# Kernel tuning notes

Measured on AMD Instinct MI355X. Metric: run time of the kernel, lower is better.

Reference implementation:

```python
import jax, jax.numpy as jnp
import numpy as np

N_NODES = 100000
N_EDGES = 640000
N_GRAPHS = 512
NODE_IN, EDGE_IN, HID, L = 64, 16, 128, 4
BN_EPS = 1e-5


def setup_inputs() -> dict:
    key = jax.random.key(0)
    ks = jax.random.split(key, 20)
    inp = {
        "x": jax.random.normal(ks[0], (N_NODES, NODE_IN), jnp.float32),
        "edge_index": jax.random.randint(ks[1], (2, N_EDGES), 0, N_NODES, jnp.int64 if jax.config.jax_enable_x64 else jnp.int32),
        "edge_attr": jax.random.normal(ks[2], (N_EDGES, EDGE_IN), jnp.float32),
        "batch": jnp.sort(jax.random.randint(ks[3], (N_NODES,), 0, N_GRAPHS)),
        # projections
        "node_w": jax.random.normal(ks[4], (NODE_IN, HID), jnp.float32) / np.sqrt(NODE_IN),
        "node_b": jnp.zeros((HID,), jnp.float32),
        "edge_w": jax.random.normal(ks[5], (EDGE_IN, HID), jnp.float32) / np.sqrt(EDGE_IN),
        "edge_b": jnp.zeros((HID,), jnp.float32),
        # per-layer GINE MLP: Linear(HID,2H) -> ReLU -> Linear(2H,HID)
        "w1": jax.random.normal(ks[6], (L, HID, 2 * HID), jnp.float32) / np.sqrt(HID),
        "b1": jnp.zeros((L, 2 * HID), jnp.float32),
        "w2": jax.random.normal(ks[7], (L, 2 * HID, HID), jnp.float32) / np.sqrt(2 * HID),
        "b2": jnp.zeros((L, HID), jnp.float32),
        # batchnorm affine params
        "gamma": jnp.ones((L, HID), jnp.float32),
        "beta": jnp.zeros((L, HID), jnp.float32),
    }
    return inp


def reference(x, edge_index, edge_attr, batch, node_w, node_b, edge_w, edge_b,
              w1, b1, w2, b2, gamma, beta):
    n = x.shape[0]
    h = jax.nn.relu(x @ node_w + node_b)              # [N, H]
    e = jax.nn.relu(edge_attr @ edge_w + edge_b)      # [E, H]
    src, dst = edge_index[0], edge_index[1]
    for l in range(L):
        # GINEConv: msg = relu(x_src + edge_attr); sum-aggregate at dst; eps = 0
        msg = jax.nn.relu(h[src] + e)                 # [E, H]
        agg = jax.ops.segment_sum(msg, dst, num_segments=n)
        z = h + agg                                   # (1+eps)*x + aggr
        z = jax.nn.relu(z @ w1[l] + b1[l]) @ w2[l] + b2[l]
        # BatchNorm1d (training-mode batch stats, biased var)
        mean = jnp.mean(z, axis=0)
        var = jnp.var(z, axis=0)
        z = (z - mean) * jax.lax.rsqrt(var + BN_EPS) * gamma[l] + beta[l]
        h = jax.nn.relu(z)                            # dropout is identity at eval
    # global mean pool over graphs
    sums = jax.ops.segment_sum(h, batch, num_segments=N_GRAPHS)
    cnt = jax.ops.segment_sum(jnp.ones((n,), h.dtype), batch, num_segments=N_GRAPHS)
    return sums / jnp.maximum(cnt, 1.0)[:, None]      # [G, H]
```

## Files before the change

kernel.cpp:

```cpp
#include <hip/hip_runtime.h>
#include <hip/hip_bf16.h>

#define NN 100000
#define NE 640000
#define NG 512
#define NIN 64
#define EIN 16
#define H 128
#define H2 256
#define NL 4

__global__ __launch_bounds__(256) void k_node_proj(const float* __restrict__ x,
                                                   const float* __restrict__ W,
                                                   const float* __restrict__ b,
                                                   float* __restrict__ h) {
    __shared__ float sW[NIN * H];
    int tid = threadIdx.x;
    for (int i = tid; i < NIN * H; i += 256) sW[i] = W[i];
    __syncthreads();
    int c = tid & 127, half = tid >> 7;
    for (int node = blockIdx.x * 2 + half; node < NN; node += gridDim.x * 2) {
        const float* xr = x + (size_t)node * NIN;
        float acc = b[c];
#pragma unroll
        for (int k = 0; k < NIN; ++k) acc = fmaf(xr[k], sW[k * H + c], acc);
        h[(size_t)node * H + c] = fmaxf(acc, 0.f);
    }
}

__global__ __launch_bounds__(256) void k_hist(const int* __restrict__ dst, int* __restrict__ deg) {
    int e = blockIdx.x * 256 + threadIdx.x;
    if (e < NE) atomicAdd(&deg[dst[e]], 1);
}

__global__ __launch_bounds__(256) void k_scan1(const int* __restrict__ deg, int* __restrict__ ex,
                                               int* __restrict__ totals) {
    __shared__ int s[256];
    int t = threadIdx.x, b = blockIdx.x;
    int base = b * 1024 + t * 4;
    int v0 = (base + 0 < NN) ? deg[base + 0] : 0;
    int v1 = (base + 1 < NN) ? deg[base + 1] : 0;
    int v2 = (base + 2 < NN) ? deg[base + 2] : 0;
    int v3 = (base + 3 < NN) ? deg[base + 3] : 0;
    int t0 = v0, t1 = t0 + v1, t2 = t1 + v2, tsum = t2 + v3;
    s[t] = tsum;
    __syncthreads();
#pragma unroll
    for (int d = 1; d < 256; d <<= 1) {
        int add = (t >= d) ? s[t - d] : 0;
        __syncthreads();
        s[t] += add;
        __syncthreads();
    }
    int excl = s[t] - tsum;
    ex[base + 0] = excl;
    ex[base + 1] = excl + t0;
    ex[base + 2] = excl + t1;
    ex[base + 3] = excl + t2;
    if (t == 255) totals[b] = s[t];
}

__global__ void k_scan2(const int* __restrict__ totals, int* __restrict__ boff) {
    __shared__ int s[256];
    int t = threadIdx.x;
    int v = (t < 98) ? totals[t] : 0;
    s[t] = v;
    __syncthreads();
#pragma unroll
    for (int d = 1; d < 256; d <<= 1) {
        int add = (t >= d) ? s[t - d] : 0;
        __syncthreads();
        s[t] += add;
        __syncthreads();
    }
    if (t < 98) boff[t] = s[t] - v;
}

__global__ __launch_bounds__(256) void k_scan3(const int* __restrict__ ex, const int* __restrict__ boff,
                                               int* __restrict__ rowptr, int* __restrict__ cursor) {
    int i = blockIdx.x * 256 + threadIdx.x;
    if (i < NN) {
        int r = ex[i] + boff[i >> 10];
        rowptr[i] = r;
        cursor[i] = r;
    }
    if (i == 0) rowptr[NN] = NE;
}

__global__ __launch_bounds__(256) void k_scatter(const int* __restrict__ dst, int* __restrict__ cursor,
                                                 int* __restrict__ eids) {
    int e = blockIdx.x * 256 + threadIdx.x;
    if (e < NE) {
        int p = atomicAdd(&cursor[dst[e]], 1);
        eids[p] = e;
    }
}

__global__ void k_prm_id(float* __restrict__ prm) {
    int c = threadIdx.x;
    prm[c] = 1.f;
    prm[H + c] = 0.f;
}

__global__ __launch_bounds__(256) void k_agg(const int* __restrict__ rowptr, const int* __restrict__ eids,
                                             const int* __restrict__ src, const float* __restrict__ ea,
                                             const float* __restrict__ We, const float* __restrict__ be,
                                             const float* __restrict__ hsrc, const float* __restrict__ prm,
                                             float* __restrict__ agg) {
    int tid = threadIdx.x;
    int c = tid & 127, grp = tid >> 7;
    float wcol[EIN];
#pragma unroll
    for (int k = 0; k < EIN; ++k) wcol[k] = We[k * H + c];
    float bec = be[c], sc = prm[c], sh = prm[H + c];
    int nb = blockIdx.x * 8;
#pragma unroll
    for (int rep = 0; rep < 4; ++rep) {
        int n = nb + rep * 2 + grp;
        int s0 = rowptr[n], s1 = rowptr[n + 1];
        float acc = 0.f;
        for (int idx = s0; idx < s1; ++idx) {
            int eid = eids[idx];
            int sv = src[eid];
            const float4* ear = (const float4*)(ea + (size_t)eid * EIN);
            float4 e0 = ear[0], e1 = ear[1], e2 = ear[2], e3 = ear[3];
            float p = bec;
            p = fmaf(e0.x, wcol[0], p);  p = fmaf(e0.y, wcol[1], p);
            p = fmaf(e0.z, wcol[2], p);  p = fmaf(e0.w, wcol[3], p);
            p = fmaf(e1.x, wcol[4], p);  p = fmaf(e1.y, wcol[5], p);
            p = fmaf(e1.z, wcol[6], p);  p = fmaf(e1.w, wcol[7], p);
            p = fmaf(e2.x, wcol[8], p);  p = fmaf(e2.y, wcol[9], p);
            p = fmaf(e2.z, wcol[10], p); p = fmaf(e2.w, wcol[11], p);
            p = fmaf(e3.x, wcol[12], p); p = fmaf(e3.y, wcol[13], p);
            p = fmaf(e3.z, wcol[14], p); p = fmaf(e3.w, wcol[15], p);
            p = fmaxf(p, 0.f);
            float hv = hsrc[(size_t)sv * H + c];
            hv = fmaxf(fmaf(sc, hv, sh), 0.f);
            acc += fmaxf(hv + p, 0.f);
        }
        agg[(size_t)n * H + c] = acc;
    }
}

__global__ __launch_bounds__(256) void k_mlp(const float* __restrict__ hsrc,
                                             const float* __restrict__ prm,
                                             float* __restrict__ agg,
                                             const float* __restrict__ w1,
                                             const float* __restrict__ b1,
                                             const float* __restrict__ w2,
                                             const float* __restrict__ b2,
                                             float* __restrict__ stats) {
    __shared__ float sz[32 * H];
    __shared__ float st[32 * H2];
    __shared__ float ls[2 * H];
    int tid = threadIdx.x;
    int base = blockIdx.x * 32;
    ls[tid < 256 ? tid : 0] = 0.f;

    float4* sz4 = (float4*)sz;
    const float4* X4 = (const float4*)hsrc;
    const float4* A4 = (const float4*)agg;
#pragma unroll
    for (int it = 0; it < 4; ++it) {
        int chunk = tid + it * 256;
        int n = chunk >> 5;
        int c4 = (chunk & 31);
        const float4 sc4 = *(const float4*)&prm[c4 * 4];
        const float4 sh4 = *(const float4*)&prm[H + c4 * 4];
        size_t gi = (size_t)(base + n) * 32 + c4;
        float4 hv = X4[gi], av = A4[gi];
        float4 z;
        z.x = fmaxf(fmaf(sc4.x, hv.x, sh4.x), 0.f) + av.x;
        z.y = fmaxf(fmaf(sc4.y, hv.y, sh4.y), 0.f) + av.y;
        z.z = fmaxf(fmaf(sc4.z, hv.z, sh4.z), 0.f) + av.z;
        z.w = fmaxf(fmaf(sc4.w, hv.w, sh4.w), 0.f) + av.w;
        sz4[chunk] = z;
    }
    __syncthreads();

    {
        int c64 = tid & 63, ng = tid >> 6;
        const float4* W14 = (const float4*)w1;
        float4 acc[8];
        float4 b1v = *(const float4*)&b1[c64 * 4];
#pragma unroll
        for (int n = 0; n < 8; ++n) acc[n] = b1v;
        for (int k0 = 0; k0 < H; k0 += 4) {
            float4 wv0 = W14[(k0 + 0) * 64 + c64];
            float4 wv1 = W14[(k0 + 1) * 64 + c64];
            float4 wv2 = W14[(k0 + 2) * 64 + c64];
            float4 wv3 = W14[(k0 + 3) * 64 + c64];
#pragma unroll
            for (int n = 0; n < 8; ++n) {
                float4 zv = sz4[(ng * 8 + n) * 32 + (k0 >> 2)];
                acc[n].x = fmaf(zv.x, wv0.x, acc[n].x); acc[n].y = fmaf(zv.x, wv0.y, acc[n].y);
                acc[n].z = fmaf(zv.x, wv0.z, acc[n].z); acc[n].w = fmaf(zv.x, wv0.w, acc[n].w);
                acc[n].x = fmaf(zv.y, wv1.x, acc[n].x); acc[n].y = fmaf(zv.y, wv1.y, acc[n].y);
                acc[n].z = fmaf(zv.y, wv1.z, acc[n].z); acc[n].w = fmaf(zv.y, wv1.w, acc[n].w);
                acc[n].x = fmaf(zv.z, wv2.x, acc[n].x); acc[n].y = fmaf(zv.z, wv2.y, acc[n].y);
                acc[n].z = fmaf(zv.z, wv2.z, acc[n].z); acc[n].w = fmaf(zv.z, wv2.w, acc[n].w);
                acc[n].x = fmaf(zv.w, wv3.x, acc[n].x); acc[n].y = fmaf(zv.w, wv3.y, acc[n].y);
                acc[n].z = fmaf(zv.w, wv3.z, acc[n].z); acc[n].w = fmaf(zv.w, wv3.w, acc[n].w);
            }
        }
        float4* st4 = (float4*)st;
#pragma unroll
        for (int n = 0; n < 8; ++n) {
            float4 r;
            r.x = fmaxf(acc[n].x, 0.f); r.y = fmaxf(acc[n].y, 0.f);
            r.z = fmaxf(acc[n].z, 0.f); r.w = fmaxf(acc[n].w, 0.f);
            st4[(ng * 8 + n) * 64 + c64] = r;
        }
    }
    __syncthreads();

    {
        int c32 = tid & 31, ng = tid >> 5;
        const float4* W24 = (const float4*)w2;
        const float4* st4 = (const float4*)st;
        float4 acc2[4];
        float4 b2v = *(const float4*)&b2[c32 * 4];
#pragma unroll
        for (int n = 0; n < 4; ++n) acc2[n] = b2v;
        for (int j0 = 0; j0 < H2; j0 += 4) {
            float4 wv0 = W24[(j0 + 0) * 32 + c32];
            float4 wv1 = W24[(j0 + 1) * 32 + c32];
            float4 wv2 = W24[(j0 + 2) * 32 + c32];
            float4 wv3 = W24[(j0 + 3) * 32 + c32];
#pragma unroll
            for (int n = 0; n < 4; ++n) {
                float4 tv = st4[(ng * 4 + n) * 64 + (j0 >> 2)];
                acc2[n].x = fmaf(tv.x, wv0.x, acc2[n].x); acc2[n].y = fmaf(tv.x, wv0.y, acc2[n].y);
                acc2[n].z = fmaf(tv.x, wv0.z, acc2[n].z); acc2[n].w = fmaf(tv.x, wv0.w, acc2[n].w);
                acc2[n].x = fmaf(tv.y, wv1.x, acc2[n].x); acc2[n].y = fmaf(tv.y, wv1.y, acc2[n].y);
                acc2[n].z = fmaf(tv.y, wv1.z, acc2[n].z); acc2[n].w = fmaf(tv.y, wv1.w, acc2[n].w);
                acc2[n].x = fmaf(tv.z, wv2.x, acc2[n].x); acc2[n].y = fmaf(tv.z, wv2.y, acc2[n].y);
                acc2[n].z = fmaf(tv.z, wv2.z, acc2[n].z); acc2[n].w = fmaf(tv.z, wv2.w, acc2[n].w);
                acc2[n].x = fmaf(tv.w, wv3.x, acc2[n].x); acc2[n].y = fmaf(tv.w, wv3.y, acc2[n].y);
                acc2[n].z = fmaf(tv.w, wv3.z, acc2[n].z); acc2[n].w = fmaf(tv.w, wv3.w, acc2[n].w);
            }
        }
        float4* O4 = (float4*)agg;
        float4 sv = {0, 0, 0, 0}, qv = {0, 0, 0, 0};
#pragma unroll
        for (int n = 0; n < 4; ++n) {
            O4[(size_t)(base + ng * 4 + n) * 32 + c32] = acc2[n];
            sv.x += acc2[n].x; sv.y += acc2[n].y; sv.z += acc2[n].z; sv.w += acc2[n].w;
            qv.x += acc2[n].x * acc2[n].x; qv.y += acc2[n].y * acc2[n].y;
            qv.z += acc2[n].z * acc2[n].z; qv.w += acc2[n].w * acc2[n].w;
        }
        int cb = c32 * 4;
        atomicAdd(&ls[cb + 0], sv.x); atomicAdd(&ls[cb + 1], sv.y);
        atomicAdd(&ls[cb + 2], sv.z); atomicAdd(&ls[cb + 3], sv.w);
        atomicAdd(&ls[H + cb + 0], qv.x); atomicAdd(&ls[H + cb + 1], qv.y);
        atomicAdd(&ls[H + cb + 2], qv.z); atomicAdd(&ls[H + cb + 3], qv.w);
    }
    __syncthreads();
    if (tid < 256) atomicAdd(&stats[tid], ls[tid]);
}

__global__ void k_bn_fin(const float* __restrict__ stats, const float* __restrict__ gamma,
                         const float* __restrict__ beta, float* __restrict__ prm) {
    int c = threadIdx.x;
    float mean = stats[c] * (1.f / NN);
    float var = stats[H + c] * (1.f / NN) - mean * mean;
    float sc = gamma[c] * rsqrtf(var + 1e-5f);
    prm[c] = sc;
    prm[H + c] = beta[c] - mean * sc;
}

__global__ __launch_bounds__(256) void k_pool(const float* __restrict__ z2, const float* __restrict__ prm,
                                              const int* __restrict__ batch, float* __restrict__ sums,
                                              float* __restrict__ cntf) {
    int tid = threadIdx.x;
    int c = tid & 127, half = tid >> 7;
    float sc = prm[c], sh = prm[H + c];
    int n0 = blockIdx.x * 64 + half * 32;
    float acc = 0.f;
    int curg = -1, runlen = 0;
    for (int i = 0; i < 32; ++i) {
        int n = n0 + i;
        if (n >= NN) break;
        int g = batch[n];
        float v = fmaxf(fmaf(sc, z2[(size_t)n * H + c], sh), 0.f);
        if (g != curg) {
            if (curg >= 0) {
                atomicAdd(&sums[(size_t)curg * H + c], acc);
                if (c == 0) atomicAdd(&cntf[curg], (float)runlen);
            }
            curg = g; acc = v; runlen = 1;
        } else {
            acc += v; runlen++;
        }
    }
    if (curg >= 0) {
        atomicAdd(&sums[(size_t)curg * H + c], acc);
        if (c == 0) atomicAdd(&cntf[curg], (float)runlen);
    }
}

__global__ void k_pool_fin(const float* __restrict__ sums, const float* __restrict__ cntf,
                           float* __restrict__ out) {
    int i = blockIdx.x * blockDim.x + threadIdx.x;
    if (i < NG * H) {
        int g = i >> 7;
        out[i] = sums[i] / fmaxf(cntf[g], 1.f);
    }
}

extern "C" void kernel_launch(void* const* d_in, const int* in_sizes, int n_in,
                              void* d_out, int out_size, void* d_ws, size_t ws_size,
                              hipStream_t stream) {
    const float* x      = (const float*)d_in[0];
    const int*   ei     = (const int*)d_in[1];
    const float* ea     = (const float*)d_in[2];
    const int*   batch  = (const int*)d_in[3];
    const float* node_w = (const float*)d_in[4];
    const float* node_b = (const float*)d_in[5];
    const float* edge_w = (const float*)d_in[6];
    const float* edge_b = (const float*)d_in[7];
    const float* w1     = (const float*)d_in[8];
    const float* b1     = (const float*)d_in[9];
    const float* w2     = (const float*)d_in[10];
    const float* b2     = (const float*)d_in[11];
    const float* gamma  = (const float*)d_in[12];
    const float* beta   = (const float*)d_in[13];
    float* out = (float*)d_out;

    char* ws = (char*)d_ws;
    const size_t SZ_H = (size_t)NN * H * 4;
    float* X     = (float*)(ws);
    float* Y     = (float*)(ws + SZ_H);
    char*  tail  = ws + 2 * SZ_H;
    float* stats = (float*)(tail);
    float* prm   = (float*)(tail + 1024);
    float* pool  = (float*)(tail + 1024 + 8192);
    float* cntf  = (float*)(tail + 1024 + 8192 + 262144);
    char*  itail = tail + 1024 + 8192 + 262144 + 2048;
    int* deg    = (int*)(itail);
    int* ex     = deg + 100352;
    int* totals = ex + 100352;
    int* boff   = totals + 128;
    int* rowptr = boff + 128;
    int* cursor = rowptr + 100352;
    int* eids   = cursor + 100352;

    const int* srcp = ei;
    const int* dstp = ei + NE;

    hipMemsetAsync(deg, 0, 100352 * sizeof(int), stream);
    k_hist<<<2500, 256, 0, stream>>>(dstp, deg);
    k_scan1<<<98, 256, 0, stream>>>(deg, ex, totals);
    k_scan2<<<1, 256, 0, stream>>>(totals, boff);
    k_scan3<<<392, 256, 0, stream>>>(ex, boff, rowptr, cursor);
    k_scatter<<<2500, 256, 0, stream>>>(dstp, cursor, eids);

    k_prm_id<<<1, 128, 0, stream>>>(prm);
    k_node_proj<<<2048, 256, 0, stream>>>(x, node_w, node_b, X);

    float* hs = X;
    float* ag = Y;
    for (int l = 0; l < NL; ++l) {
        hipMemsetAsync(stats, 0, 256 * sizeof(float), stream);
        k_agg<<<12500, 256, 0, stream>>>(rowptr, eids, srcp, ea, edge_w, edge_b,
                                         hs, prm + l * 256, ag);
        k_mlp<<<3125, 256, 0, stream>>>(hs, prm + l * 256, ag,
                                        w1 + (size_t)l * H * H2, b1 + (size_t)l * H2,
                                        w2 + (size_t)l * H2 * H, b2 + (size_t)l * H, stats);
        k_bn_fin<<<1, 128, 0, stream>>>(stats, gamma + (size_t)l * H, beta + (size_t)l * H,
                                        prm + (l + 1) * 256);
        float* tmp = hs; hs = ag; ag = tmp;
    }

    hipMemsetAsync(pool, 0, (NG * H + NG) * sizeof(float), stream);
    k_pool<<<1563, 256, 0, stream>>>(hs, prm + NL * 256, batch, pool, cntf);
    k_pool_fin<<<256, 256, 0, stream>>>(pool, cntf, out);
}
```

Measured before the change: 2.081 ms.

## Edge-balanced segmented aggregation with packed edge records and retiled MLP

Aggregation now splits the sorted edge list into fixed 32-edge chunks per thread group instead of walking one node's adjacency list at a time. This evens out load across degree-skewed nodes, and per-destination partial sums are flushed with atomics. Edge records now pack src, dst and edge id into one int4, removing the dependent eids→src load chain. Loads are batched four edges at a time to raise memory-level parallelism. The cost is an extra memset of the aggregation buffer each layer plus atomic traffic. The MLP kernel is also retiled so each thread covers 8 output columns, and the hidden tile is padded to avoid LDS bank conflicts.

```diff
diff --git a/kernel.cpp b/kernel.cpp
--- a/kernel.cpp
+++ b/kernel.cpp
@@ -9,6 +9,12 @@
 #define H 128
 #define H2 256
 #define NL 4
+
+#define FMA4(acc, s, wv)                      \
+    acc.x = fmaf(s, wv.x, acc.x);             \
+    acc.y = fmaf(s, wv.y, acc.y);             \
+    acc.z = fmaf(s, wv.z, acc.z);             \
+    acc.w = fmaf(s, wv.w, acc.w)
 
 __global__ __launch_bounds__(256) void k_node_proj(const float* __restrict__ x,
                                                    const float* __restrict__ W,
@@ -87,12 +93,15 @@
     if (i == 0) rowptr[NN] = NE;
 }
 
-__global__ __launch_bounds__(256) void k_scatter(const int* __restrict__ dst, int* __restrict__ cursor,
-                                                 int* __restrict__ eids) {
+__global__ __launch_bounds__(256) void k_scatter(const int* __restrict__ src,
+                                                 const int* __restrict__ dst,
+                                                 int* __restrict__ cursor,
+                                                 int4* __restrict__ erec) {
     int e = blockIdx.x * 256 + threadIdx.x;
     if (e < NE) {
-        int p = atomicAdd(&cursor[dst[e]], 1);
-        eids[p] = e;
+        int d = dst[e];
+        int p = atomicAdd(&cursor[d], 1);
+        erec[p] = make_int4(src[e], d, e, 0);
     }
 }
 
@@ -102,10 +111,12 @@
     prm[H + c] = 0.f;
 }
 
-__global__ __launch_bounds__(256) void k_agg(const int* __restrict__ rowptr, const int* __restrict__ eids,
-                                             const int* __restrict__ src, const float* __restrict__ ea,
-                                             const float* __restrict__ We, const float* __restrict__ be,
-                                             const float* __restrict__ hsrc, const float* __restrict__ prm,
+__global__ __launch_bounds__(256) void k_agg(const int4* __restrict__ erec,
+                                             const float* __restrict__ ea,
+                                             const float* __restrict__ We,
+                                             const float* __restrict__ be,
+                                             const float* __restrict__ hsrc,
+                                             const float* __restrict__ prm,
                                              float* __restrict__ agg) {
     int tid = threadIdx.x;
     int c = tid & 127, grp = tid >> 7;
@@ -113,35 +124,65 @@
 #pragma unroll
     for (int k = 0; k < EIN; ++k) wcol[k] = We[k * H + c];
     float bec = be[c], sc = prm[c], sh = prm[H + c];
-    int nb = blockIdx.x * 8;
-#pragma unroll
-    for (int rep = 0; rep < 4; ++rep) {
-        int n = nb + rep * 2 + grp;
-        int s0 = rowptr[n], s1 = rowptr[n + 1];
-        float acc = 0.f;
-        for (int idx = s0; idx < s1; ++idx) {
-            int eid = eids[idx];
-            int sv = src[eid];
-            const float4* ear = (const float4*)(ea + (size_t)eid * EIN);
-            float4 e0 = ear[0], e1 = ear[1], e2 = ear[2], e3 = ear[3];
-            float p = bec;
-            p = fmaf(e0.x, wcol[0], p);  p = fmaf(e0.y, wcol[1], p);
-            p = fmaf(e0.z, wcol[2], p);  p = fmaf(e0.w, wcol[3], p);
-            p = fmaf(e1.x, wcol[4], p);  p = fmaf(e1.y, wcol[5], p);
-            p = fmaf(e1.z, wcol[6], p);  p = fmaf(e1.w, wcol[7], p);
-            p = fmaf(e2.x, wcol[8], p);  p = fmaf(e2.y, wcol[9], p);
-            p = fmaf(e2.z, wcol[10], p); p = fmaf(e2.w, wcol[11], p);
-            p = fmaf(e3.x, wcol[12], p); p = fmaf(e3.y, wcol[13], p);
-            p = fmaf(e3.z, wcol[14], p); p = fmaf(e3.w, wcol[15], p);
-            p = fmaxf(p, 0.f);
-            float hv = hsrc[(size_t)sv * H + c];
-            hv = fmaxf(fmaf(sc, hv, sh), 0.f);
-            acc += fmaxf(hv + p, 0.f);
-        }
-        agg[(size_t)n * H + c] = acc;
-    }
-}
-
+    const float4* ea4 = (const float4*)ea;
+    int base = (blockIdx.x * 2 + grp) * 32;
+    int cur = erec[base].y;
+    float acc = 0.f;
+#pragma unroll 2
+    for (int i0 = 0; i0 < 32; i0 += 4) {
+        int4 r0 = erec[base + i0 + 0];
+        int4 r1 = erec[base + i0 + 1];
+        int4 r2 = erec[base + i0 + 2];
+        int4 r3 = erec[base + i0 + 3];
+        float hv0 = hsrc[(size_t)r0.x * H + c];
+        float hv1 = hsrc[(size_t)r1.x * H + c];
+        float hv2 = hsrc[(size_t)r2.x * H + c];
+        float hv3 = hsrc[(size_t)r3.x * H + c];
+        float4 a0 = ea4[(size_t)r0.z * 4 + 0], a1 = ea4[(size_t)r0.z * 4 + 1],
+               a2 = ea4[(size_t)r0.z * 4 + 2], a3 = ea4[(size_t)r0.z * 4 + 3];
+        float4 b0 = ea4[(size_t)r1.z * 4 + 0], b1 = ea4[(size_t)r1.z * 4 + 1],
+               b2 = ea4[(size_t)r1.z * 4 + 2], b3 = ea4[(size_t)r1.z * 4 + 3];
+        float4 c0 = ea4[(size_t)r2.z * 4 + 0], c1 = ea4[(size_t)r2.z * 4 + 1],
+               c2 = ea4[(size_t)r2.z * 4 + 2], c3 = ea4[(size_t)r2.z * 4 + 3];
+        float4 d0 = ea4[(size_t)r3.z * 4 + 0], d1 = ea4[(size_t)r3.z * 4 + 1],
+               d2 = ea4[(size_t)r3.z * 4 + 2], d3 = ea4[(size_t)r3.z * 4 + 3];
+
+#define EPROJ(pp, e0, e1, e2, e3)                                              \
+        {                                                                      \
+            pp = bec;                                                          \
+            pp = fmaf(e0.x, wcol[0], pp);  pp = fmaf(e0.y, wcol[1], pp);       \
+            pp = fmaf(e0.z, wcol[2], pp);  pp = fmaf(e0.w, wcol[3], pp);       \
+            pp = fmaf(e1.x, wcol[4], pp);  pp = fmaf(e1.y, wcol[5], pp);       \
+            pp = fmaf(e1.z, wcol[6], pp);  pp = fmaf(e1.w, wcol[7], pp);       \
+            pp = fmaf(e2.x, wcol[8], pp);  pp = fmaf(e2.y, wcol[9], pp);       \
+            pp = fmaf(e2.z, wcol[10], pp); pp = fmaf(e2.w, wcol[11], pp);      \
+            pp = fmaf(e3.x, wcol[12], pp); pp = fmaf(e3.y, wcol[13], pp);      \
+            pp = fmaf(e3.z, wcol[14], pp); pp = fmaf(e3.w, wcol[15], pp);      \
+            pp = fmaxf(pp, 0.f);                                               \
+        }
+        float p0, p1, p2, p3;
+        EPROJ(p0, a0, a1, a2, a3)
+        EPROJ(p1, b0, b1, b2, b3)
+        EPROJ(p2, c0, c1, c2, c3)
+        EPROJ(p3, d0, d1, d2, d3)
+#undef EPROJ
+        float m0 = fmaxf(fmaxf(fmaf(sc, hv0, sh), 0.f) + p0, 0.f);
+        float m1 = fmaxf(fmaxf(fmaf(sc, hv1, sh), 0.f) + p1, 0.f);
+        float m2 = fmaxf(fmaxf(fmaf(sc, hv2, sh), 0.f) + p2, 0.f);
+        float m3 = fmaxf(fmaxf(fmaf(sc, hv3, sh), 0.f) + p3, 0.f);
+        if (r0.y != cur) { atomicAdd(&agg[(size_t)cur * H + c], acc); acc = 0.f; cur = r0.y; }
+        acc += m0;
+        if (r1.y != cur) { atomicAdd(&agg[(size_t)cur * H + c], acc); acc = 0.f; cur = r1.y; }
+        acc += m1;
+        if (r2.y != cur) { atomicAdd(&agg[(size_t)cur * H + c], acc); acc = 0.f; cur = r2.y; }
+        acc += m2;
+        if (r3.y != cur) { atomicAdd(&agg[(size_t)cur * H + c], acc); acc = 0.f; cur = r3.y; }
+        acc += m3;
+    }
+    atomicAdd(&agg[(size_t)cur * H + c], acc);
+}
+
+#define STP 65
 __global__ __launch_bounds__(256) void k_mlp(const float* __restrict__ hsrc,
                                              const float* __restrict__ prm,
                                              float* __restrict__ agg,
@@ -150,21 +191,20 @@
                                              const float* __restrict__ w2,
                                              const float* __restrict__ b2,
                                              float* __restrict__ stats) {
-    __shared__ float sz[32 * H];
-    __shared__ float st[32 * H2];
+    __shared__ float4 sz4[32 * 32];
+    __shared__ float4 st4[32 * STP];
     __shared__ float ls[2 * H];
     int tid = threadIdx.x;
     int base = blockIdx.x * 32;
-    ls[tid < 256 ? tid : 0] = 0.f;
-
-    float4* sz4 = (float4*)sz;
+    ls[tid] = 0.f;
+
     const float4* X4 = (const float4*)hsrc;
     const float4* A4 = (const float4*)agg;
 #pragma unroll
     for (int it = 0; it < 4; ++it) {
         int chunk = tid + it * 256;
         int n = chunk >> 5;
-        int c4 = (chunk & 31);
+        int c4 = chunk & 31;
         const float4 sc4 = *(const float4*)&prm[c4 * 4];
         const float4 sh4 = *(const float4*)&prm[H + c4 * 4];
         size_t gi = (size_t)(base + n) * 32 + c4;
@@ -179,84 +219,85 @@
     __syncthreads();
 
     {
-        int c64 = tid & 63, ng = tid >> 6;
+        int cg = tid & 31, ng = tid >> 5;
         const float4* W14 = (const float4*)w1;
-        float4 acc[8];
-        float4 b1v = *(const float4*)&b1[c64 * 4];
-#pragma unroll
-        for (int n = 0; n < 8; ++n) acc[n] = b1v;
+        float4 accA[4], accB[4];
+        float4 bA = ((const float4*)b1)[cg * 2], bB = ((const float4*)b1)[cg * 2 + 1];
+#pragma unroll
+        for (int n = 0; n < 4; ++n) { accA[n] = bA; accB[n] = bB; }
         for (int k0 = 0; k0 < H; k0 += 4) {
-            float4 wv0 = W14[(k0 + 0) * 64 + c64];
-            float4 wv1 = W14[(k0 + 1) * 64 + c64];
-            float4 wv2 = W14[(k0 + 2) * 64 + c64];
-            float4 wv3 = W14[(k0 + 3) * 64 + c64];
-#pragma unroll
-            for (int n = 0; n < 8; ++n) {
-                float4 zv = sz4[(ng * 8 + n) * 32 + (k0 >> 2)];
-                acc[n].x = fmaf(zv.x, wv0.x, acc[n].x); acc[n].y = fmaf(zv.x, wv0.y, acc[n].y);
-                acc[n].z = fmaf(zv.x, wv0.z, acc[n].z); acc[n].w = fmaf(zv.x, wv0.w, acc[n].w);
-                acc[n].x = fmaf(zv.y, wv1.x, acc[n].x); acc[n].y = fmaf(zv.y, wv1.y, acc[n].y);
-                acc[n].z = fmaf(zv.y, wv1.z, acc[n].z); acc[n].w = fmaf(zv.y, wv1.w, acc[n].w);
-                acc[n].x = fmaf(zv.z, wv2.x, acc[n].x); acc[n].y = fmaf(zv.z, wv2.y, acc[n].y);
-                acc[n].z = fmaf(zv.z, wv2.z, acc[n].z); acc[n].w = fmaf(zv.z, wv2.w, acc[n].w);
-                acc[n].x = fmaf(zv.w, wv3.x, acc[n].x); acc[n].y = fmaf(zv.w, wv3.y, acc[n].y);
-                acc[n].z = fmaf(zv.w, wv3.z, acc[n].z); acc[n].w = fmaf(zv.w, wv3.w, acc[n].w);
+            float4 w0a = W14[(k0 + 0) * 64 + cg * 2], w0b = W14[(k0 + 0) * 64 + cg * 2 + 1];
+            float4 w1a = W14[(k0 + 1) * 64 + cg * 2], w1b = W14[(k0 + 1) * 64 + cg * 2 + 1];
+            float4 w2a = W14[(k0 + 2) * 64 + cg * 2], w2b = W14[(k0 + 2) * 64 + cg * 2 + 1];
+            float4 w3a = W14[(k0 + 3) * 64 + cg * 2], w3b = W14[(k0 + 3) * 64 + cg * 2 + 1];
+#pragma unroll
+            for (int n = 0; n < 4; ++n) {
+                float4 zv = sz4[(ng * 4 + n) * 32 + (k0 >> 2)];
+                FMA4(accA[n], zv.x, w0a); FMA4(accB[n], zv.x, w0b);
+                FMA4(accA[n], zv.y, w1a); FMA4(accB[n], zv.y, w1b);
+                FMA4(accA[n], zv.z, w2a); FMA4(accB[n], zv.z, w2b);
+                FMA4(accA[n], zv.w, w3a); FMA4(accB[n], zv.w, w3b);
             }
         }
-        float4* st4 = (float4*)st;
-#pragma unroll
-        for (int n = 0; n < 8; ++n) {
-            float4 r;
-            r.x = fmaxf(acc[n].x, 0.f); r.y = fmaxf(acc[n].y, 0.f);
-            r.z = fmaxf(acc[n].z, 0.f); r.w = fmaxf(acc[n].w, 0.f);
-            st4[(ng * 8 + n) * 64 + c64] = r;
+#pragma unroll
+        for (int n = 0; n < 4; ++n) {
+            float4 rA, rB;
+            rA.x = fmaxf(accA[n].x, 0.f); rA.y = fmaxf(accA[n].y, 0.f);
+            rA.z = fmaxf(accA[n].z, 0.f); rA.w = fmaxf(accA[n].w, 0.f);
+            rB.x = fmaxf(accB[n].x, 0.f); rB.y = fmaxf(accB[n].y, 0.f);
+            rB.z = fmaxf(accB[n].z, 0.f); rB.w = fmaxf(accB[n].w, 0.f);
+            st4[(ng * 4 + n) * STP + cg * 2] = rA;
+            st4[(ng * 4 + n) * STP + cg * 2 + 1] = rB;
         }
     }
     __syncthreads();
 
     {
-        int c32 = tid & 31, ng = tid >> 5;
+        int cg = tid & 15, ng = tid >> 4;
         const float4* W24 = (const float4*)w2;
-        const float4* st4 = (const float4*)st;
-        float4 acc2[4];
-        float4 b2v = *(const float4*)&b2[c32 * 4];
-#pragma unroll
-        for (int n = 0; n < 4; ++n) acc2[n] = b2v;
+        float4 aA[2], aB[2];
+        float4 bA = ((const float4*)b2)[cg * 2], bB = ((const float4*)b2)[cg * 2 + 1];
+#pragma unroll
+        for (int n = 0; n < 2; ++n) { aA[n] = bA; aB[n] = bB; }
         for (int j0 = 0; j0 < H2; j0 += 4) {
-            float4 wv0 = W24[(j0 + 0) * 32 + c32];
-            float4 wv1 = W24[(j0 + 1) * 32 + c32];
-            float4 wv2 = W24[(j0 + 2) * 32 + c32];
-            float4 wv3 = W24[(j0 + 3) * 32 + c32];
-#pragma unroll
-            for (int n = 0; n < 4; ++n) {
-                float4 tv = st4[(ng * 4 + n) * 64 + (j0 >> 2)];
-                acc2[n].x = fmaf(tv.x, wv0.x, acc2[n].x); acc2[n].y = fmaf(tv.x, wv0.y, acc2[n].y);
-                acc2[n].z = fmaf(tv.x, wv0.z, acc2[n].z); acc2[n].w = fmaf(tv.x, wv0.w, acc2[n].w);
-                acc2[n].x = fmaf(tv.y, wv1.x, acc2[n].x); acc2[n].y = fmaf(tv.y, wv1.y, acc2[n].y);
-                acc2[n].z = fmaf(tv.y, wv1.z, acc2[n].z); acc2[n].w = fmaf(tv.y, wv1.w, acc2[n].w);
-                acc2[n].x = fmaf(tv.z, wv2.x, acc2[n].x); acc2[n].y = fmaf(tv.z, wv2.y, acc2[n].y);
-                acc2[n].z = fmaf(tv.z, wv2.z, acc2[n].z); acc2[n].w = fmaf(tv.z, wv2.w, acc2[n].w);
-                acc2[n].x = fmaf(tv.w, wv3.x, acc2[n].x); acc2[n].y = fmaf(tv.w, wv3.y, acc2[n].y);
-                acc2[n].z = fmaf(tv.w, wv3.z, acc2[n].z); acc2[n].w = fmaf(tv.w, wv3.w, acc2[n].w);
+            float4 w0a = W24[(j0 + 0) * 32 + cg * 2], w0b = W24[(j0 + 0) * 32 + cg * 2 + 1];
+            float4 w1a = W24[(j0 + 1) * 32 + cg * 2], w1b = W24[(j0 + 1) * 32 + cg * 2 + 1];
+            float4 w2a = W24[(j0 + 2) * 32 + cg * 2], w2b = W24[(j0 + 2) * 32 + cg * 2 + 1];
+            float4 w3a = W24[(j0 + 3) * 32 + cg * 2], w3b = W24[(j0 + 3) * 32 + cg * 2 + 1];
+#pragma unroll
+            for (int n = 0; n < 2; ++n) {
+                float4 tv = st4[(ng * 2 + n) * STP + (j0 >> 2)];
+                FMA4(aA[n], tv.x, w0a); FMA4(aB[n], tv.x, w0b);
+                FMA4(aA[n], tv.y, w1a); FMA4(aB[n], tv.y, w1b);
+                FMA4(aA[n], tv.z, w2a); FMA4(aB[n], tv.z, w2b);
+                FMA4(aA[n], tv.w, w3a); FMA4(aB[n], tv.w, w3b);
             }
         }
         float4* O4 = (float4*)agg;
-        float4 sv = {0, 0, 0, 0}, qv = {0, 0, 0, 0};
-#pragma unroll
-        for (int n = 0; n < 4; ++n) {
-            O4[(size_t)(base + ng * 4 + n) * 32 + c32] = acc2[n];
-            sv.x += acc2[n].x; sv.y += acc2[n].y; sv.z += acc2[n].z; sv.w += acc2[n].w;
-            qv.x += acc2[n].x * acc2[n].x; qv.y += acc2[n].y * acc2[n].y;
-            qv.z += acc2[n].z * acc2[n].z; qv.w += acc2[n].w * acc2[n].w;
-        }
-        int cb = c32 * 4;
-        atomicAdd(&ls[cb + 0], sv.x); atomicAdd(&ls[cb + 1], sv.y);
-        atomicAdd(&ls[cb + 2], sv.z); atomicAdd(&ls[cb + 3], sv.w);
-        atomicAdd(&ls[H + cb + 0], qv.x); atomicAdd(&ls[H + cb + 1], qv.y);
-        atomicAdd(&ls[H + cb + 2], qv.z); atomicAdd(&ls[H + cb + 3], qv.w);
-    }
-    __syncthreads();
-    if (tid < 256) atomicAdd(&stats[tid], ls[tid]);
+        float4 svA = {0, 0, 0, 0}, svB = {0, 0, 0, 0}, qvA = {0, 0, 0, 0}, qvB = {0, 0, 0, 0};
+#pragma unroll
+        for (int n = 0; n < 2; ++n) {
+            O4[(size_t)(base + ng * 2 + n) * 32 + cg * 2] = aA[n];
+            O4[(size_t)(base + ng * 2 + n) * 32 + cg * 2 + 1] = aB[n];
+            svA.x += aA[n].x; svA.y += aA[n].y; svA.z += aA[n].z; svA.w += aA[n].w;
+            svB.x += aB[n].x; svB.y += aB[n].y; svB.z += aB[n].z; svB.w += aB[n].w;
+            qvA.x += aA[n].x * aA[n].x; qvA.y += aA[n].y * aA[n].y;
+            qvA.z += aA[n].z * aA[n].z; qvA.w += aA[n].w * aA[n].w;
+            qvB.x += aB[n].x * aB[n].x; qvB.y += aB[n].y * aB[n].y;
+            qvB.z += aB[n].z * aB[n].z; qvB.w += aB[n].w * aB[n].w;
+        }
+        int cb = cg * 8;
+        atomicAdd(&ls[cb + 0], svA.x); atomicAdd(&ls[cb + 1], svA.y);
+        atomicAdd(&ls[cb + 2], svA.z); atomicAdd(&ls[cb + 3], svA.w);
+        atomicAdd(&ls[cb + 4], svB.x); atomicAdd(&ls[cb + 5], svB.y);
+        atomicAdd(&ls[cb + 6], svB.z); atomicAdd(&ls[cb + 7], svB.w);
+        atomicAdd(&ls[H + cb + 0], qvA.x); atomicAdd(&ls[H + cb + 1], qvA.y);
+        atomicAdd(&ls[H + cb + 2], qvA.z); atomicAdd(&ls[H + cb + 3], qvA.w);
+        atomicAdd(&ls[H + cb + 4], qvB.x); atomicAdd(&ls[H + cb + 5], qvB.y);
+        atomicAdd(&ls[H + cb + 6], qvB.z); atomicAdd(&ls[H + cb + 7], qvB.w);
+    }
+    __syncthreads();
+    atomicAdd(&stats[tid], ls[tid]);
 }
 
 __global__ void k_bn_fin(const float* __restrict__ stats, const float* __restrict__ gamma,
@@ -337,13 +378,13 @@
     float* pool  = (float*)(tail + 1024 + 8192);
     float* cntf  = (float*)(tail + 1024 + 8192 + 262144);
     char*  itail = tail + 1024 + 8192 + 262144 + 2048;
-    int* deg    = (int*)(itail);
-    int* ex     = deg + 100352;
-    int* totals = ex + 100352;
-    int* boff   = totals + 128;
-    int* rowptr = boff + 128;
-    int* cursor = rowptr + 100352;
-    int* eids   = cursor + 100352;
+    int4* erec   = (int4*)(itail);
+    int*  deg    = (int*)(itail + (size_t)NE * 16);
+    int*  ex     = deg + 100352;
+    int*  totals = ex + 100352;
+    int*  boff   = totals + 128;
+    int*  rowptr = boff + 128;
+    int*  cursor = rowptr + 100352;
 
     const int* srcp = ei;
     const int* dstp = ei + NE;
@@ -353,7 +394,7 @@
     k_scan1<<<98, 256, 0, stream>>>(deg, ex, totals);
     k_scan2<<<1, 256, 0, stream>>>(totals, boff);
     k_scan3<<<392, 256, 0, stream>>>(ex, boff, rowptr, cursor);
-    k_scatter<<<2500, 256, 0, stream>>>(dstp, cursor, eids);
+    k_scatter<<<2500, 256, 0, stream>>>(srcp, dstp, cursor, erec);
 
     k_prm_id<<<1, 128, 0, stream>>>(prm);
     k_node_proj<<<2048, 256, 0, stream>>>(x, node_w, node_b, X);
@@ -361,9 +402,9 @@
     float* hs = X;
     float* ag = Y;
     for (int l = 0; l < NL; ++l) {
+        hipMemsetAsync(ag, 0, SZ_H, stream);
         hipMemsetAsync(stats, 0, 256 * sizeof(float), stream);
-        k_agg<<<12500, 256, 0, stream>>>(rowptr, eids, srcp, ea, edge_w, edge_b,
-                                         hs, prm + l * 256, ag);
+        k_agg<<<10000, 256, 0, stream>>>(erec, ea, edge_w, edge_b, hs, prm + l * 256, ag);
         k_mlp<<<3125, 256, 0, stream>>>(hs, prm + l * 256, ag,
                                         w1 + (size_t)l * H * H2, b1 + (size_t)l * H2,
                                         w2 + (size_t)l * H2 * H, b2 + (size_t)l * H, stats);
```

Measured after the change: 2.598 ms. 1.25x slower.
